# Kernel tuning notes

Hardware: AMD Instinct MI355X
Metric: run time of the kernel (lower is better)

## Reference

```python
import jax, jax.numpy as jnp
import numpy as np

N = 50000      # nodes per object type (2 types)
F = 128        # input feature dim (num_feat)
H = 64         # FLAGS.hidden1 == FLAGS.hidden2
E = 800000     # edges per relation
NET = 4        # edge types: (0,0),(0,1),(1,0),(1,1); for k: dst type i=k//2, src type j=k%2


def setup_inputs() -> dict:
    key = jax.random.key(0)
    ks = jax.random.split(key, 7)
    x0 = jax.random.normal(ks[0], (N, F), jnp.float32)
    x1 = jax.random.normal(ks[1], (N, F), jnp.float32)
    src = jax.random.randint(ks[2], (NET, E), 0, N, jnp.int32)
    dst = jax.random.randint(ks[3], (NET, E), 0, N, jnp.int32)
    # normalized adjacency values (~1/avg_degree keeps activations stable)
    ew = jax.random.uniform(ks[4], (NET, E), jnp.float32) / 16.0
    W1 = jax.random.normal(ks[5], (NET, F, H), jnp.float32) / np.sqrt(F).astype(np.float32)
    Wl = jax.random.normal(ks[6], (NET, NET, H, H), jnp.float32) / np.sqrt(H).astype(np.float32)
    return {"x0": x0, "x1": x1, "src": src, "dst": dst, "ew": ew, "W1": W1, "Wl": Wl}


def _spmm(src_k, dst_k, w_k, x):
    # sparse [N_i, N_j] adjacency @ dense x: gather + weighted scatter-add
    return jax.ops.segment_sum(w_k[:, None] * x[src_k], dst_k, num_segments=N)


def _layer(xs, Ws, src, dst, ew, relu):
    # xs: [x_type0, x_type1]; per edge type (i,j): out[i] += A_ij @ (x_j @ W_ij)
    outs = [jnp.zeros((N, Ws.shape[-1]), xs[0].dtype) for _ in range(2)]
    for k in range(NET):
        i, j = k // 2, k % 2
        outs[i] = outs[i] + _spmm(src[k], dst[k], ew[k], xs[j] @ Ws[k])
    if relu:
        outs = [jax.nn.relu(o) for o in outs]
    return outs


def reference(x0, x1, src, dst, ew, W1, Wl):
    h1 = _layer([x0, x1], W1, src, dst, ew, relu=True)       # hidden1
    e1 = _layer(h1, Wl[0], src, dst, ew, relu=True)          # embeddings1
    e2 = _layer(e1, Wl[1], src, dst, ew, relu=True)          # embeddings2
    e3 = _layer(e2, Wl[2], src, dst, ew, relu=True)          # embeddings3
    emb = _layer(e3, Wl[3], src, dst, ew, relu=False)        # embeddings = add_n(reltyp4), no relu
    # final concat per object type: [hidden1, embeddings1, embeddings] -> (N, 3H)
    return jnp.stack([jnp.concatenate([h1[t], e1[t], emb[t]], axis=1) for t in range(2)])
```

## Files before the change

kernel.cpp:

```cpp
#include <hip/hip_runtime.h>
#include <cstddef>

#define NREL 4
#define NSUP 2
#define HD 64
#define FD 128
#define BSHIFT 8
#define BUCKET 256
#define CHUNK 16384

static inline int idiv_up(int a, int b) { return (a + b - 1) / b; }

typedef __attribute__((ext_vector_type(8))) short bf16x8;
typedef __attribute__((ext_vector_type(4))) float f32x4;

__device__ __forceinline__ unsigned short f2bf(float f) {
    unsigned int u = __float_as_uint(f);
    unsigned int r = (u + 0x7FFFu + ((u >> 16) & 1u)) >> 16;
    return (unsigned short)r;
}
__device__ __forceinline__ float bflo(unsigned int v) {
    return __uint_as_float(v << 16);
}
__device__ __forceinline__ float bfhi(unsigned int v) {
    return __uint_as_float(v & 0xFFFF0000u);
}
__device__ __forceinline__ unsigned int cvtpk_bf16(float lo, float hi) {
    unsigned int r;
    asm("v_cvt_pk_bf16_f32 %0, %1, %2" : "=v"(r) : "v"(lo), "v"(hi));
    return r;
}


__global__ void pcount_kernel(const int* __restrict__ dst, int* __restrict__ ccnt,
                              int E2, int NBP, int NCH) {
    int k = blockIdx.y;
    int c = blockIdx.x;
    extern __shared__ int lh[];
    for (int i = threadIdx.x; i < NBP; i += blockDim.x) lh[i] = 0;
    __syncthreads();
    const int* dk = dst + (size_t)k * E2;
    int base = c * CHUNK;
    int n = min(CHUNK, E2 - base);
    for (int i = threadIdx.x; i < n; i += blockDim.x)
        atomicAdd(&lh[dk[base + i] >> BSHIFT], 1);
    __syncthreads();
    int* out = ccnt + ((size_t)k * NCH + c) * NBP;
    for (int i = threadIdx.x; i < NBP; i += blockDim.x) out[i] = lh[i];
}


__global__ void pscan_kernel(int* __restrict__ ccnt, int* __restrict__ bptr,
                             int NBP, int NCH, int E2) {
    int k = blockIdx.x;
    int tid = threadIdx.x;
    int* cc = ccnt + (size_t)k * NCH * NBP;
    int total = 0;
    if (tid < NBP) {
        for (int c = 0; c < NCH; ++c) {
            int v = cc[c * NBP + tid];
            cc[c * NBP + tid] = total;
            total += v;
        }
    }
    __shared__ int wsum[4];
    int wid = tid >> 6, lane = tid & 63;
    int x = total;
    #pragma unroll
    for (int off = 1; off < 64; off <<= 1) {
        int y = __shfl_up(x, off, 64);
        if (lane >= off) x += y;
    }
    if (lane == 63) wsum[wid] = x;
    __syncthreads();
    if (tid == 0) {
        int s = 0;
        #pragma unroll
        for (int j = 0; j < 4; ++j) { int t = wsum[j]; wsum[j] = s; s += t; }
    }
    __syncthreads();
    int excl = x - total + wsum[wid];
    if (tid < NBP) bptr[(size_t)k * (NBP + 1) + tid] = excl;
    if (tid == 0) bptr[(size_t)k * (NBP + 1) + NBP] = E2;
}


__global__ void pplace_kernel(const int* __restrict__ src, const int* __restrict__ dst,
                              const float* __restrict__ ew, const int* __restrict__ ccnt,
                              const int* __restrict__ bptr, int2* __restrict__ staged,
                              int E, int E2, int N, int NBP, int NCH) {
    int k = blockIdx.y;
    int c = blockIdx.x;
    extern __shared__ int sh[];
    int* lcnt = sh;
    int* lbase = sh + NBP;
    const int* cc = ccnt + ((size_t)k * NCH + c) * NBP;
    for (int i = threadIdx.x; i < NBP; i += blockDim.x) {
        lbase[i] = bptr[(size_t)k * (NBP + 1) + i] + cc[i];
        lcnt[i] = 0;
    }
    __syncthreads();
    const int* sk = src + (size_t)k * E2;
    const int* dk = dst + (size_t)k * E2;
    const float* wk = ew + (size_t)k * E2;
    int base = c * CHUNK;
    int n = min(CHUNK, E2 - base);
    int2* out = staged + (size_t)k * E2;
    for (int i = threadIdx.x; i < n; i += blockDim.x) {
        int gi = base + i;
        int d = dk[gi];
        int b = d >> BSHIFT;
        int row = sk[gi] + ((gi >= E) ? N : 0);
        int local = atomicAdd(&lcnt[b], 1);
        out[lbase[b] + local] =
            make_int2(row | ((d & (BUCKET - 1)) << 17), __float_as_int(wk[gi]));
    }
}


__global__ void bsort_kernel(const int2* __restrict__ staged, const int* __restrict__ bptr,
                             int* __restrict__ rowptr, unsigned int* __restrict__ edges,
                             int E2, int N, int NBP) {
    int k = blockIdx.y;
    int b = blockIdx.x;
    __shared__ int hist[BUCKET];
    __shared__ int excl[BUCKET];
    __shared__ int cur[BUCKET];
    __shared__ int wsum2[4];
    int tid = threadIdx.x;
    int wid = tid >> 6, lane = tid & 63;
    if (tid < BUCKET) hist[tid] = 0;
    __syncthreads();
    int beg = bptr[(size_t)k * (NBP + 1) + b];
    int end = bptr[(size_t)k * (NBP + 1) + b + 1];
    const int2* in = staged + (size_t)k * E2;
    for (int i = beg + tid; i < end; i += blockDim.x)
        atomicAdd(&hist[(in[i].x >> 17) & (BUCKET - 1)], 1);
    __syncthreads();
    int v = 0, x = 0;
    if (tid < BUCKET) {
        v = hist[tid];
        x = v;
        #pragma unroll
        for (int off = 1; off < 64; off <<= 1) {
            int y = __shfl_up(x, off, 64);
            if (lane >= off) x += y;
        }
        if (lane == 63) wsum2[wid] = x;
    }
    __syncthreads();
    if (tid == 0) {
        int s = 0;
        #pragma unroll
        for (int j = 0; j < 4; ++j) { int t = wsum2[j]; wsum2[j] = s; s += t; }
    }
    __syncthreads();
    if (tid < BUCKET) {
        int e = x - v + wsum2[wid];
        excl[tid] = e;
        cur[tid] = e;
    }
    __syncthreads();
    unsigned int* outp = edges + (size_t)k * E2;
    for (int i = beg + tid; i < end; i += blockDim.x) {
        int2 q = in[i];
        int dl = (q.x >> 17) & (BUCKET - 1);
        int pos = atomicAdd(&cur[dl], 1);
        unsigned int wb = (unsigned int)(f2bf(__int_as_float(q.y)) & 0x7FFF);
        outp[beg + pos] = ((unsigned int)q.x & 0x1FFFFu) | (wb << 17);
    }
    int node0 = b * BUCKET;
    if (tid < BUCKET && node0 + tid < N)
        rowptr[(size_t)k * (N + 1) + node0 + tid] = beg + excl[tid];
    if (b == 0 && tid == 0) rowptr[(size_t)k * (N + 1) + N] = E2;
}


__global__ void convw_kernel(const float* __restrict__ W, unsigned short* __restrict__ Wf,
                             int mats, int KK) {
    int tid = blockIdx.x * blockDim.x + threadIdx.x;
    int total = mats * KK * 4 * 64;
    if (tid >= total) return;
    int l = tid & 63;
    int n = (tid >> 6) & 3;
    int rest = tid >> 8;
    int kk = rest % KK;
    int mat = rest / KK;
    int h = l >> 4, c = l & 15;
    int K = KK * 32;
    const float* Wm = W + (size_t)mat * K * 64;
    unsigned short* o = Wf + (size_t)tid * 8;
    #pragma unroll
    for (int i = 0; i < 8; ++i)
        o[i] = f2bf(Wm[(size_t)(kk * 32 + h * 8 + i) * 64 + n * 16 + c]);
}


template <int K>
__global__ void gemm_mfma_kernel(const unsigned short* __restrict__ Xb,
                                 const unsigned short* __restrict__ Wf,
                                 unsigned short* __restrict__ Ybase, int N) {
    constexpr int KK = K / 32;
    int rel = blockIdx.y;
    const unsigned short* X = Xb + (size_t)(rel & 1) * N * K;
    const bf16x8* Wv = reinterpret_cast<const bf16x8*>(Wf + (size_t)rel * KK * 4 * 64 * 8);
    unsigned short* Y = Ybase + (size_t)rel * N * HD;
    int tid = threadIdx.x;
    int w = tid >> 6, l = tid & 63;
    int lr = l & 15, lh = l >> 4;
    int row0 = blockIdx.x * 128 + w * 32;
    f32x4 acc00 = {0.f,0.f,0.f,0.f}, acc01 = {0.f,0.f,0.f,0.f};
    f32x4 acc02 = {0.f,0.f,0.f,0.f}, acc03 = {0.f,0.f,0.f,0.f};
    f32x4 acc10 = {0.f,0.f,0.f,0.f}, acc11 = {0.f,0.f,0.f,0.f};
    f32x4 acc12 = {0.f,0.f,0.f,0.f}, acc13 = {0.f,0.f,0.f,0.f};
    int r0 = min(row0 + lr, N - 1);
    int r1 = min(row0 + 16 + lr, N - 1);
    const unsigned short* xp0 = X + (size_t)r0 * K + lh * 8;
    const unsigned short* xp1 = X + (size_t)r1 * K + lh * 8;
    #pragma unroll
    for (int kk = 0; kk < KK; ++kk) {
        bf16x8 a0 = *reinterpret_cast<const bf16x8*>(xp0 + kk * 32);
        bf16x8 a1 = *reinterpret_cast<const bf16x8*>(xp1 + kk * 32);
        bf16x8 b0 = Wv[(kk * 4 + 0) * 64 + l];
        bf16x8 b1 = Wv[(kk * 4 + 1) * 64 + l];
        bf16x8 b2 = Wv[(kk * 4 + 2) * 64 + l];
        bf16x8 b3 = Wv[(kk * 4 + 3) * 64 + l];
        acc00 = __builtin_amdgcn_mfma_f32_16x16x32_bf16(a0, b0, acc00, 0, 0, 0);
        acc01 = __builtin_amdgcn_mfma_f32_16x16x32_bf16(a0, b1, acc01, 0, 0, 0);
        acc02 = __builtin_amdgcn_mfma_f32_16x16x32_bf16(a0, b2, acc02, 0, 0, 0);
        acc03 = __builtin_amdgcn_mfma_f32_16x16x32_bf16(a0, b3, acc03, 0, 0, 0);
        acc10 = __builtin_amdgcn_mfma_f32_16x16x32_bf16(a1, b0, acc10, 0, 0, 0);
        acc11 = __builtin_amdgcn_mfma_f32_16x16x32_bf16(a1, b1, acc11, 0, 0, 0);
        acc12 = __builtin_amdgcn_mfma_f32_16x16x32_bf16(a1, b2, acc12, 0, 0, 0);
        acc13 = __builtin_amdgcn_mfma_f32_16x16x32_bf16(a1, b3, acc13, 0, 0, 0);
    }
    #pragma unroll
    for (int reg = 0; reg < 4; ++reg) {
        int rowa = row0 + lh * 4 + reg;
        if (rowa < N) {
            unsigned short* yp = Y + (size_t)rowa * HD + lr;
            yp[0]  = f2bf(acc00[reg]);
            yp[16] = f2bf(acc01[reg]);
            yp[32] = f2bf(acc02[reg]);
            yp[48] = f2bf(acc03[reg]);
        }
        int rowb = row0 + 16 + lh * 4 + reg;
        if (rowb < N) {
            unsigned short* yp = Y + (size_t)rowb * HD + lr;
            yp[0]  = f2bf(acc10[reg]);
            yp[16] = f2bf(acc11[reg]);
            yp[32] = f2bf(acc12[reg]);
            yp[48] = f2bf(acc13[reg]);
        }
    }
}


__global__ void gemm_mfma_f32in_kernel(const float* __restrict__ X0,
                                       const float* __restrict__ X1,
                                       const unsigned short* __restrict__ Wf,
                                       unsigned short* __restrict__ Ybase, int N) {
    constexpr int K = FD;
    constexpr int KK = K / 32;
    int rel = blockIdx.y;
    const float* X = (rel & 1) ? X1 : X0;
    const bf16x8* Wv = reinterpret_cast<const bf16x8*>(Wf + (size_t)rel * KK * 4 * 64 * 8);
    unsigned short* Y = Ybase + (size_t)rel * N * HD;
    int tid = threadIdx.x;
    int w = tid >> 6, l = tid & 63;
    int lr = l & 15, lh = l >> 4;
    int row0 = blockIdx.x * 128 + w * 32;
    f32x4 acc00 = {0.f,0.f,0.f,0.f}, acc01 = {0.f,0.f,0.f,0.f};
    f32x4 acc02 = {0.f,0.f,0.f,0.f}, acc03 = {0.f,0.f,0.f,0.f};
    f32x4 acc10 = {0.f,0.f,0.f,0.f}, acc11 = {0.f,0.f,0.f,0.f};
    f32x4 acc12 = {0.f,0.f,0.f,0.f}, acc13 = {0.f,0.f,0.f,0.f};
    int r0 = min(row0 + lr, N - 1);
    int r1 = min(row0 + 16 + lr, N - 1);
    const float* xp0 = X + (size_t)r0 * K + lh * 8;
    const float* xp1 = X + (size_t)r1 * K + lh * 8;
    #pragma unroll
    for (int kk = 0; kk < KK; ++kk) {
        float4 xa0 = *reinterpret_cast<const float4*>(xp0 + kk * 32);
        float4 xa1 = *reinterpret_cast<const float4*>(xp0 + kk * 32 + 4);
        float4 xb0 = *reinterpret_cast<const float4*>(xp1 + kk * 32);
        float4 xb1 = *reinterpret_cast<const float4*>(xp1 + kk * 32 + 4);
        union { unsigned int u[4]; bf16x8 v; } ca, cb;
        ca.u[0] = cvtpk_bf16(xa0.x, xa0.y);
        ca.u[1] = cvtpk_bf16(xa0.z, xa0.w);
        ca.u[2] = cvtpk_bf16(xa1.x, xa1.y);
        ca.u[3] = cvtpk_bf16(xa1.z, xa1.w);
        cb.u[0] = cvtpk_bf16(xb0.x, xb0.y);
        cb.u[1] = cvtpk_bf16(xb0.z, xb0.w);
        cb.u[2] = cvtpk_bf16(xb1.x, xb1.y);
        cb.u[3] = cvtpk_bf16(xb1.z, xb1.w);
        bf16x8 a0 = ca.v;
        bf16x8 a1 = cb.v;
        bf16x8 b0 = Wv[(kk * 4 + 0) * 64 + l];
        bf16x8 b1 = Wv[(kk * 4 + 1) * 64 + l];
        bf16x8 b2 = Wv[(kk * 4 + 2) * 64 + l];
        bf16x8 b3 = Wv[(kk * 4 + 3) * 64 + l];
        acc00 = __builtin_amdgcn_mfma_f32_16x16x32_bf16(a0, b0, acc00, 0, 0, 0);
        acc01 = __builtin_amdgcn_mfma_f32_16x16x32_bf16(a0, b1, acc01, 0, 0, 0);
        acc02 = __builtin_amdgcn_mfma_f32_16x16x32_bf16(a0, b2, acc02, 0, 0, 0);
        acc03 = __builtin_amdgcn_mfma_f32_16x16x32_bf16(a0, b3, acc03, 0, 0, 0);
        acc10 = __builtin_amdgcn_mfma_f32_16x16x32_bf16(a1, b0, acc10, 0, 0, 0);
        acc11 = __builtin_amdgcn_mfma_f32_16x16x32_bf16(a1, b1, acc11, 0, 0, 0);
        acc12 = __builtin_amdgcn_mfma_f32_16x16x32_bf16(a1, b2, acc12, 0, 0, 0);
        acc13 = __builtin_amdgcn_mfma_f32_16x16x32_bf16(a1, b3, acc13, 0, 0, 0);
    }
    #pragma unroll
    for (int reg = 0; reg < 4; ++reg) {
        int rowa = row0 + lh * 4 + reg;
        if (rowa < N) {
            unsigned short* yp = Y + (size_t)rowa * HD + lr;
            yp[0]  = f2bf(acc00[reg]);
            yp[16] = f2bf(acc01[reg]);
            yp[32] = f2bf(acc02[reg]);
            yp[48] = f2bf(acc03[reg]);
        }
        int rowb = row0 + 16 + lh * 4 + reg;
        if (rowb < N) {
            unsigned short* yp = Y + (size_t)rowb * HD + lr;
            yp[0]  = f2bf(acc10[reg]);
            yp[16] = f2bf(acc11[reg]);
            yp[32] = f2bf(acc12[reg]);
            yp[48] = f2bf(acc13[reg]);
        }
    }
}


__global__ void spmm_kernel(const unsigned short* __restrict__ Ybase,
                            const int* __restrict__ rowptr, const unsigned int* __restrict__ edges,
                            unsigned short* __restrict__ act, float* __restrict__ outp,
                            int N, int E2, int relu) {
    int id = blockIdx.x;
    int g = id & 7;
    int t = g >> 2;
    int pbi = (id >> 3) * 4 + (g & 3);
    int wave = threadIdx.x >> 6;
    int lane = threadIdx.x & 63;
    int d = pbi * 4 + wave;
    if (d >= N) return;
    int h = lane >> 4;
    int c4 = (lane & 15) * 4;
    const unsigned short* Y = Ybase + (size_t)(2 * t) * N * HD;
    const unsigned int* ep = edges + (size_t)t * E2;
    int beg = rowptr[(size_t)t * (N + 1) + d];
    int end = rowptr[(size_t)t * (N + 1) + d + 1];
    float4 a0 = {0.f,0.f,0.f,0.f}, a1 = {0.f,0.f,0.f,0.f};
    float4 a2 = {0.f,0.f,0.f,0.f}, a3 = {0.f,0.f,0.f,0.f};
    if (beg < end) {
        int endm1 = end - 1;
        unsigned int m0, m1, m2, m3;
        {
            int i0 = beg + 0 + h, i1 = beg + 4 + h, i2 = beg + 8 + h, i3 = beg + 12 + h;
            m0 = ep[i0 < end ? i0 : endm1];
            m1 = ep[i1 < end ? i1 : endm1];
            m2 = ep[i2 < end ? i2 : endm1];
            m3 = ep[i3 < end ? i3 : endm1];
        }
        for (int base = beg; ; ) {
            int nb = base + 16;
            bool more = nb < end;
            unsigned int n0, n1, n2, n3;
            if (more) {
                int i0 = nb + 0 + h, i1 = nb + 4 + h, i2 = nb + 8 + h, i3 = nb + 12 + h;
                n0 = ep[i0 < end ? i0 : endm1];
                n1 = ep[i1 < end ? i1 : endm1];
                n2 = ep[i2 < end ? i2 : endm1];
                n3 = ep[i3 < end ? i3 : endm1];
            }
            uint2 y0 = *reinterpret_cast<const uint2*>(Y + ((m0 & 0x1FFFFu) * HD + c4));
            uint2 y1 = *reinterpret_cast<const uint2*>(Y + ((m1 & 0x1FFFFu) * HD + c4));
            uint2 y2 = *reinterpret_cast<const uint2*>(Y + ((m2 & 0x1FFFFu) * HD + c4));
            uint2 y3 = *reinterpret_cast<const uint2*>(Y + ((m3 & 0x1FFFFu) * HD + c4));
            float w0 = ((base + 0 + h) < end) ? __uint_as_float((m0 >> 17) << 16) : 0.f;
            float w1 = ((base + 4 + h) < end) ? __uint_as_float((m1 >> 17) << 16) : 0.f;
            float w2 = ((base + 8 + h) < end) ? __uint_as_float((m2 >> 17) << 16) : 0.f;
            float w3 = ((base + 12 + h) < end) ? __uint_as_float((m3 >> 17) << 16) : 0.f;
            a0.x += w0 * bflo(y0.x); a0.y += w0 * bfhi(y0.x);
            a0.z += w0 * bflo(y0.y); a0.w += w0 * bfhi(y0.y);
            a1.x += w1 * bflo(y1.x); a1.y += w1 * bfhi(y1.x);
            a1.z += w1 * bflo(y1.y); a1.w += w1 * bfhi(y1.y);
            a2.x += w2 * bflo(y2.x); a2.y += w2 * bfhi(y2.x);
            a2.z += w2 * bflo(y2.y); a2.w += w2 * bfhi(y2.y);
            a3.x += w3 * bflo(y3.x); a3.y += w3 * bfhi(y3.x);
            a3.z += w3 * bflo(y3.y); a3.w += w3 * bfhi(y3.y);
            if (!more) break;
            base = nb;
            m0 = n0; m1 = n1; m2 = n2; m3 = n3;
        }
    }
    float4 s;
    s.x = (a0.x + a1.x) + (a2.x + a3.x);
    s.y = (a0.y + a1.y) + (a2.y + a3.y);
    s.z = (a0.z + a1.z) + (a2.z + a3.z);
    s.w = (a0.w + a1.w) + (a2.w + a3.w);
    s.x += __shfl_xor(s.x, 16, 64);  s.x += __shfl_xor(s.x, 32, 64);
    s.y += __shfl_xor(s.y, 16, 64);  s.y += __shfl_xor(s.y, 32, 64);
    s.z += __shfl_xor(s.z, 16, 64);  s.z += __shfl_xor(s.z, 32, 64);
    s.w += __shfl_xor(s.w, 16, 64);  s.w += __shfl_xor(s.w, 32, 64);
    if (relu) {
        s.x = fmaxf(s.x, 0.f); s.y = fmaxf(s.y, 0.f);
        s.z = fmaxf(s.z, 0.f); s.w = fmaxf(s.w, 0.f);
    }
    if (lane < 16) {
        if (act) {
            ushort4 ob;
            ob.x = f2bf(s.x); ob.y = f2bf(s.y); ob.z = f2bf(s.z); ob.w = f2bf(s.w);
            *reinterpret_cast<ushort4*>(&act[((size_t)t * N + d) * HD + c4]) = ob;
        }
        if (outp) *reinterpret_cast<float4*>(&outp[((size_t)t * N + d) * 192 + c4]) = s;
    }
}


extern "C" void kernel_launch(void* const* d_in, const int* in_sizes, int n_in,
                              void* d_out, int out_size, void* d_ws, size_t ws_size,
                              hipStream_t stream) {
    const float* x0 = (const float*)d_in[0];
    const float* x1 = (const float*)d_in[1];
    const int* src = (const int*)d_in[2];
    const int* dst = (const int*)d_in[3];
    const float* ew = (const float*)d_in[4];
    const float* W1 = (const float*)d_in[5];
    const float* Wl = (const float*)d_in[6];
    float* out = (float*)d_out;

    int N = in_sizes[0] / FD;
    int E = in_sizes[2] / NREL;
    int E2 = 2 * E;
    int NBP = idiv_up(N, BUCKET);
    int NCH = idiv_up(E2, CHUNK);

    char* ws = (char*)d_ws;
    size_t off = 0;
    auto alloc = [&](size_t bytes) -> void* {
        void* p = ws + off;
        off = (off + bytes + 255) & ~(size_t)255;
        return p;
    };
    int* ccnt    = (int*)alloc((size_t)NSUP * NCH * NBP * 4);
    int* bptr    = (int*)alloc((size_t)NSUP * (NBP + 1) * 4);
    int* rowptr  = (int*)alloc((size_t)NSUP * (N + 1) * 4);
    unsigned int* edges = (unsigned int*)alloc((size_t)NSUP * E2 * 4);
    unsigned short* y    = (unsigned short*)alloc((size_t)NREL * N * HD * 2);
    unsigned short* actb = (unsigned short*)alloc((size_t)2 * N * HD * 2);
    unsigned short* W1f  = (unsigned short*)alloc((size_t)NREL * 4 * 4 * 64 * 8 * 2);
    unsigned short* Wlf  = (unsigned short*)alloc((size_t)16 * 2 * 4 * 64 * 8 * 2);
    int2* staged = (int2*)alloc((size_t)NSUP * E2 * 8);
    (void)ws_size;

    convw_kernel<<<idiv_up(NREL * 4 * 4 * 64, 256), 256, 0, stream>>>(W1, W1f, NREL, 4);
    convw_kernel<<<idiv_up(16 * 2 * 4 * 64, 256), 256, 0, stream>>>(Wl, Wlf, 16, 2);

    pcount_kernel<<<dim3(NCH, NSUP), 1024, NBP * 4, stream>>>(dst, ccnt, E2, NBP, NCH);
    pscan_kernel<<<NSUP, 256, 0, stream>>>(ccnt, bptr, NBP, NCH, E2);
    pplace_kernel<<<dim3(NCH, NSUP), 1024, 2 * NBP * 4, stream>>>(
        src, dst, ew, ccnt, bptr, staged, E, E2, N, NBP, NCH);
    bsort_kernel<<<dim3(NBP, NSUP), 1024, 0, stream>>>(staged, bptr, rowptr, edges, E2, N, NBP);

    dim3 ggrid(idiv_up(N, 128), NREL);
    int NB4 = idiv_up(N, 4);
    int sgx = idiv_up(NB4, 4) * 8;

    gemm_mfma_f32in_kernel<<<ggrid, 256, 0, stream>>>(x0, x1, W1f, y, N);
    spmm_kernel<<<sgx, 256, 0, stream>>>(y, rowptr, edges, actb, out + 0, N, E2, 1);

    for (int l = 0; l < 4; ++l) {
        gemm_mfma_kernel<HD><<<ggrid, 256, 0, stream>>>(
            actb, Wlf + (size_t)l * 4 * 2 * 4 * 64 * 8, y, N);
        float* op = (l == 0) ? (out + 64) : (l == 3) ? (out + 128) : nullptr;
        unsigned short* ap = (l == 3) ? nullptr : actb;
        int relu = (l == 3) ? 0 : 1;
        spmm_kernel<<<sgx, 256, 0, stream>>>(y, rowptr, edges, ap, op, N, E2, relu);
    }
}
```

Baseline: 425.3 us.

## Split SpMM feature columns across four blocks per destination row group

The SpMM kernel now assigns each block a 16-column slice of the 64-wide feature row. Each wave handles one destination row, with 8 lanes covering 16 columns via 4-byte loads and 8 lane-groups striding over edges. The grid grows fourfold so that more waves run in parallel and each lane's edge walk is shorter. In exchange, every edge index and weight is read four times, one per column group, and each gather becomes a narrower 4-byte load. That narrower load may use DRAM sectors less efficiently.

```diff
diff --git a/kernel.cpp b/kernel.cpp
--- a/kernel.cpp
+++ b/kernel.cpp
@@ -337,81 +337,74 @@
     int id = blockIdx.x;
     int g = id & 7;
     int t = g >> 2;
-    int pbi = (id >> 3) * 4 + (g & 3);
+    int cg = g & 3;
+    int pbi = id >> 3;
     int wave = threadIdx.x >> 6;
     int lane = threadIdx.x & 63;
     int d = pbi * 4 + wave;
     if (d >= N) return;
-    int h = lane >> 4;
-    int c4 = (lane & 15) * 4;
-    const unsigned short* Y = Ybase + (size_t)(2 * t) * N * HD;
+    int h = lane >> 3;
+    int cp = (lane & 7) * 2;
+    int coff = cg * 16 + cp;
+    const unsigned short* Y = Ybase + (size_t)(2 * t) * N * HD + coff;
     const unsigned int* ep = edges + (size_t)t * E2;
     int beg = rowptr[(size_t)t * (N + 1) + d];
     int end = rowptr[(size_t)t * (N + 1) + d + 1];
-    float4 a0 = {0.f,0.f,0.f,0.f}, a1 = {0.f,0.f,0.f,0.f};
-    float4 a2 = {0.f,0.f,0.f,0.f}, a3 = {0.f,0.f,0.f,0.f};
+    float2 a0 = {0.f,0.f}, a1 = {0.f,0.f}, a2 = {0.f,0.f}, a3 = {0.f,0.f};
     if (beg < end) {
         int endm1 = end - 1;
         unsigned int m0, m1, m2, m3;
         {
-            int i0 = beg + 0 + h, i1 = beg + 4 + h, i2 = beg + 8 + h, i3 = beg + 12 + h;
+            int i0 = beg + 0 + h, i1 = beg + 8 + h, i2 = beg + 16 + h, i3 = beg + 24 + h;
             m0 = ep[i0 < end ? i0 : endm1];
             m1 = ep[i1 < end ? i1 : endm1];
             m2 = ep[i2 < end ? i2 : endm1];
             m3 = ep[i3 < end ? i3 : endm1];
         }
         for (int base = beg; ; ) {
-            int nb = base + 16;
+            int nb = base + 32;
             bool more = nb < end;
             unsigned int n0, n1, n2, n3;
             if (more) {
-                int i0 = nb + 0 + h, i1 = nb + 4 + h, i2 = nb + 8 + h, i3 = nb + 12 + h;
+                int i0 = nb + 0 + h, i1 = nb + 8 + h, i2 = nb + 16 + h, i3 = nb + 24 + h;
                 n0 = ep[i0 < end ? i0 : endm1];
                 n1 = ep[i1 < end ? i1 : endm1];
                 n2 = ep[i2 < end ? i2 : endm1];
                 n3 = ep[i3 < end ? i3 : endm1];
             }
-            uint2 y0 = *reinterpret_cast<const uint2*>(Y + ((m0 & 0x1FFFFu) * HD + c4));
-            uint2 y1 = *reinterpret_cast<const uint2*>(Y + ((m1 & 0x1FFFFu) * HD + c4));
-            uint2 y2 = *reinterpret_cast<const uint2*>(Y + ((m2 & 0x1FFFFu) * HD + c4));
-            uint2 y3 = *reinterpret_cast<const uint2*>(Y + ((m3 & 0x1FFFFu) * HD + c4));
+            unsigned int y0 = *reinterpret_cast<const unsigned int*>(Y + (m0 & 0x1FFFFu) * HD);
+            unsigned int y1 = *reinterpret_cast<const unsigned int*>(Y + (m1 & 0x1FFFFu) * HD);
+            unsigned int y2 = *reinterpret_cast<const unsigned int*>(Y + (m2 & 0x1FFFFu) * HD);
+            unsigned int y3 = *reinterpret_cast<const unsigned int*>(Y + (m3 & 0x1FFFFu) * HD);
             float w0 = ((base + 0 + h) < end) ? __uint_as_float((m0 >> 17) << 16) : 0.f;
-            float w1 = ((base + 4 + h) < end) ? __uint_as_float((m1 >> 17) << 16) : 0.f;
-            float w2 = ((base + 8 + h) < end) ? __uint_as_float((m2 >> 17) << 16) : 0.f;
-            float w3 = ((base + 12 + h) < end) ? __uint_as_float((m3 >> 17) << 16) : 0.f;
-            a0.x += w0 * bflo(y0.x); a0.y += w0 * bfhi(y0.x);
-            a0.z += w0 * bflo(y0.y); a0.w += w0 * bfhi(y0.y);
-            a1.x += w1 * bflo(y1.x); a1.y += w1 * bfhi(y1.x);
-            a1.z += w1 * bflo(y1.y); a1.w += w1 * bfhi(y1.y);
-            a2.x += w2 * bflo(y2.x); a2.y += w2 * bfhi(y2.x);
-            a2.z += w2 * bflo(y2.y); a2.w += w2 * bfhi(y2.y);
-            a3.x += w3 * bflo(y3.x); a3.y += w3 * bfhi(y3.x);
-            a3.z += w3 * bflo(y3.y); a3.w += w3 * bfhi(y3.y);
+            float w1 = ((base + 8 + h) < end) ? __uint_as_float((m1 >> 17) << 16) : 0.f;
+            float w2 = ((base + 16 + h) < end) ? __uint_as_float((m2 >> 17) << 16) : 0.f;
+            float w3 = ((base + 24 + h) < end) ? __uint_as_float((m3 >> 17) << 16) : 0.f;
+            a0.x += w0 * bflo(y0); a0.y += w0 * bfhi(y0);
+            a1.x += w1 * bflo(y1); a1.y += w1 * bfhi(y1);
+            a2.x += w2 * bflo(y2); a2.y += w2 * bfhi(y2);
+            a3.x += w3 * bflo(y3); a3.y += w3 * bfhi(y3);
             if (!more) break;
             base = nb;
             m0 = n0; m1 = n1; m2 = n2; m3 = n3;
         }
     }
-    float4 s;
+    float2 s;
     s.x = (a0.x + a1.x) + (a2.x + a3.x);
     s.y = (a0.y + a1.y) + (a2.y + a3.y);
-    s.z = (a0.z + a1.z) + (a2.z + a3.z);
-    s.w = (a0.w + a1.w) + (a2.w + a3.w);
-    s.x += __shfl_xor(s.x, 16, 64);  s.x += __shfl_xor(s.x, 32, 64);
-    s.y += __shfl_xor(s.y, 16, 64);  s.y += __shfl_xor(s.y, 32, 64);
-    s.z += __shfl_xor(s.z, 16, 64);  s.z += __shfl_xor(s.z, 32, 64);
-    s.w += __shfl_xor(s.w, 16, 64);  s.w += __shfl_xor(s.w, 32, 64);
-    if (relu) {
-        s.x = fmaxf(s.x, 0.f); s.y = fmaxf(s.y, 0.f);
-        s.z = fmaxf(s.z, 0.f); s.w = fmaxf(s.w, 0.f);
-    }
-    if (lane < 16) {
+    s.x += __shfl_xor(s.x, 8, 64);
+    s.x += __shfl_xor(s.x, 16, 64);
+    s.x += __shfl_xor(s.x, 32, 64);
+    s.y += __shfl_xor(s.y, 8, 64);
+    s.y += __shfl_xor(s.y, 16, 64);
+    s.y += __shfl_xor(s.y, 32, 64);
+    if (relu) { s.x = fmaxf(s.x, 0.f); s.y = fmaxf(s.y, 0.f); }
+    if (lane < 8) {
         if (act) {
-            ushort4 ob;
-            ob.x = f2bf(s.x); ob.y = f2bf(s.y); ob.z = f2bf(s.z); ob.w = f2bf(s.w);
-            *reinterpret_cast<ushort4*>(&act[((size_t)t * N + d) * HD + c4]) = ob;
-        }
-        if (outp) *reinterpret_cast<float4*>(&outp[((size_t)t * N + d) * 192 + c4]) = s;
+            ushort2 ob; ob.x = f2bf(s.x); ob.y = f2bf(s.y);
+            *reinterpret_cast<ushort2*>(&act[((size_t)t * N + d) * HD + coff]) = ob;
+        }
+        if (outp) *reinterpret_cast<float2*>(&outp[((size_t)t * N + d) * 192 + coff]) = s;
     }
 }
 
@@ -462,8 +455,7 @@
     bsort_kernel<<<dim3(NBP, NSUP), 1024, 0, stream>>>(staged, bptr, rowptr, edges, E2, N, NBP);
 
     dim3 ggrid(idiv_up(N, 128), NREL);
-    int NB4 = idiv_up(N, 4);
-    int sgx = idiv_up(NB4, 4) * 8;
+    int sgx = idiv_up(N, 4) * 8;
 
     gemm_mfma_f32in_kernel<<<ggrid, 256, 0, stream>>>(x0, x1, W1f, y, N);
     spmm_kernel<<<sgx, 256, 0, stream>>>(y, rowptr, edges, actb, out + 0, N, E2, 1);
```

Measured after the change: 1.012 ms. 138% more time.
